# Performance work log

Hardware: AMD Instinct MI355X
Metric: run time of the kernel (lower is better)

## Reference

```python
import jax, jax.numpy as jnp
import numpy as np

E = 8          # num_global_experts (experts['count_per_node'])
D = 1024       # model_dim
H = 2048       # expert hidden_size
TOP_K = 2      # gate_type['k']


def setup_inputs() -> dict:
    key = jax.random.key(0)
    k_x, k_g, k_w1, k_w2 = jax.random.split(key, 4)
    B, S = 4, 2048
    inp = {
        "input": jax.random.normal(k_x, (B, S, D), dtype=jnp.float32),
        "Wg": jax.random.normal(k_g, (D, E), dtype=jnp.float32) * 0.02,
        "W1": jax.random.normal(k_w1, (E, D, H), dtype=jnp.float32) * 0.02,
        "b1": jnp.zeros((E, H), dtype=jnp.float32),
        "W2": jax.random.normal(k_w2, (E, H, D), dtype=jnp.float32) * 0.02,
        "b2": jnp.zeros((E, D), dtype=jnp.float32),
    }
    return inp


def reference(input, Wg, W1, b1, W2, b2):
    # ---- router: top-k softmax gating, gate weights normalized over top-k ----
    logits = jnp.einsum("bsd,de->bse", input, Wg)            # [B,S,E]
    probs = jax.nn.softmax(logits, axis=-1)                   # [B,S,E]
    top_vals, top_idx = jax.lax.top_k(probs, TOP_K)           # [B,S,K]
    top_vals = top_vals / jnp.sum(top_vals, axis=-1, keepdims=True)
    onehot = jax.nn.one_hot(top_idx, E, dtype=input.dtype)    # [B,S,K,E]
    mask = jnp.sum(onehot, axis=2)                            # [B,S,E] 0/1 dispatch mask (indices)
    scores = jnp.sum(onehot * top_vals[..., None], axis=2)    # [B,S,E] combine weights

    # ---- dense masked dispatch: repeat input per expert, mask non-routed tokens ----
    xm = input[None] * jnp.moveaxis(mask, -1, 0)[..., None]   # [E,B,S,D]

    # ---- per-expert 2-layer MLP (LinearExperts) ----
    h = jnp.einsum("ebsd,edh->ebsh", xm, W1) + b1[:, None, None, :]
    h = jax.nn.relu(h)                                        # [E,B,S,H]
    y = jnp.einsum("ebsh,ehd->ebsd", h, W2) + b2[:, None, None, :]

    # ---- weighted combine: sum_e expert_out * gate score ----
    out = jnp.sum(y * jnp.moveaxis(scores, -1, 0)[..., None], axis=0)  # [B,S,D]
    return out
```

## Files before the change

### kernel.cpp

```cpp
#include <hip/hip_runtime.h>
#include <hip/hip_bf16.h>

typedef __bf16 bf16x8 __attribute__((ext_vector_type(8)));
typedef __bf16 bf16x4 __attribute__((ext_vector_type(4)));
typedef float  f32x4  __attribute__((ext_vector_type(4)));

#define T_TOK    8192
#define D_DIM    1024
#define H_DIM    2048
#define E_NUM    8
#define MAX_MB   136
#define MAX_ROWS 17408

#define OFF_MBTOT   512
#define OFF_MB2E    1024
#define OFF_MBROW0  2048
#define OFF_TOPKE   4096
#define OFF_TOPKS   69632
#define OFF_TOK     135168
#define OFF_ROWIDX  204800
#define OFF_XB      (1u<<20)
#define OFF_W1T     (18u*1024*1024)
#define OFF_W2T     (50u*1024*1024)
#define OFF_HBUF    (82u*1024*1024)
#define OFF_YBUF    OFF_XB

__device__ __forceinline__ void gload_lds16(const void* g, void* l) {
    __builtin_amdgcn_global_load_lds(
        (const __attribute__((address_space(1))) void*)g,
        (__attribute__((address_space(3))) void*)l, 16, 0, 0);
}

__global__ __launch_bounds__(256) void k_router_cvt(
    const float* __restrict__ x, const float* __restrict__ Wg,
    __bf16* __restrict__ xb, int* __restrict__ topk_e, float* __restrict__ topk_s)
{
    __shared__ float wgT[E_NUM][1032];
    const int tid = threadIdx.x;
#pragma unroll
    for (int i = 0; i < 32; ++i) {
        int f = tid + i * 256;
        wgT[f & 7][f >> 3] = Wg[f];
    }
    __syncthreads();

    const int wave = tid >> 6, lane = tid & 63;
    const int t = blockIdx.x * 4 + wave;
    const float* xr = x + (size_t)t * D_DIM;
    __bf16* xbr = xb + (size_t)t * D_DIM;

    float acc[E_NUM];
#pragma unroll
    for (int e = 0; e < E_NUM; ++e) acc[e] = 0.f;

#pragma unroll
    for (int j = 0; j < 4; ++j) {
        const int d0 = lane * 4 + j * 256;
        float4 xv = *(const float4*)(xr + d0);
        bf16x4 o = { (__bf16)xv.x, (__bf16)xv.y, (__bf16)xv.z, (__bf16)xv.w };
        *(bf16x4*)(xbr + d0) = o;
#pragma unroll
        for (int e = 0; e < E_NUM; ++e) {
            float4 wv = *(const float4*)&wgT[e][d0];
            acc[e] += xv.x * wv.x + xv.y * wv.y + xv.z * wv.z + xv.w * wv.w;
        }
    }
#pragma unroll
    for (int off = 32; off >= 1; off >>= 1)
#pragma unroll
        for (int e = 0; e < E_NUM; ++e) acc[e] += __shfl_xor(acc[e], off, 64);

    if (lane == 0) {
        int e0 = 0; float v0 = acc[0];
#pragma unroll
        for (int e = 1; e < E_NUM; ++e) if (acc[e] > v0) { v0 = acc[e]; e0 = e; }
        int e1 = -1; float v1 = -1e30f;
#pragma unroll
        for (int e = 0; e < E_NUM; ++e) if (e != e0 && acc[e] > v1) { v1 = acc[e]; e1 = e; }
        float s0 = 1.f / (1.f + __expf(v1 - v0));
        float s1 = 1.f - s0;
        topk_e[t*2+0] = e0; topk_e[t*2+1] = e1;
        topk_s[t*2+0] = s0; topk_s[t*2+1] = s1;
    }
}

#define SORT_T 256
__global__ __launch_bounds__(512) void k_sort(
    const int* __restrict__ topk_e,
    int* __restrict__ mbTot, int* __restrict__ mb2e, int* __restrict__ mbrow0,
    int* __restrict__ tok, int* __restrict__ rowidx)
{
    __shared__ int lcnt[E_NUM][SORT_T];
    __shared__ int base[E_NUM];
    __shared__ int etot[E_NUM];
    const int tid = threadIdx.x;

    if (tid < SORT_T) {
#pragma unroll
        for (int e = 0; e < E_NUM; ++e) lcnt[e][tid] = 0;
    }
    __syncthreads();

    if (tid < SORT_T) {
        const int4* p = (const int4*)(topk_e + tid * 64);
#pragma unroll
        for (int i = 0; i < 16; ++i) {
            int4 v = p[i];
            lcnt[v.x][tid]++; lcnt[v.y][tid]++; lcnt[v.z][tid]++; lcnt[v.w][tid]++;
        }
    }
    __syncthreads();

    {
        const int w = tid >> 6, l = tid & 63;
        int v0 = lcnt[w][l*4+0], v1 = lcnt[w][l*4+1], v2 = lcnt[w][l*4+2], v3 = lcnt[w][l*4+3];
        int s = v0 + v1 + v2 + v3;
        int inc = s;
#pragma unroll
        for (int off = 1; off < 64; off <<= 1) {
            int o = __shfl_up(inc, off, 64);
            if (l >= off) inc += o;
        }
        int exc = inc - s;
        lcnt[w][l*4+0] = exc;
        lcnt[w][l*4+1] = exc + v0;
        lcnt[w][l*4+2] = exc + v0 + v1;
        lcnt[w][l*4+3] = exc + v0 + v1 + v2;
        if (l == 63) etot[w] = inc;
    }
    __syncthreads();

    if (tid == 0) {
        int row = 0, mb = 0;
        for (int e = 0; e < E_NUM; ++e) {
            base[e] = row;
            int nb = (etot[e] + 127) >> 7;
            for (int b = 0; b < nb; ++b) { mb2e[mb] = e; mbrow0[mb] = row + b*128; ++mb; }
            row += nb * 128;
        }
        mbTot[0] = mb;
    }
    __syncthreads();

    if (tid < SORT_T) {
#pragma unroll
        for (int e = 0; e < E_NUM; ++e) lcnt[e][tid] += base[e];
        const int4* p = (const int4*)(topk_e + tid * 64);
#pragma unroll
        for (int i = 0; i < 16; ++i) {
            int4 v = p[i];
            int j0 = tid * 64 + i * 4;
            int r;
            r = lcnt[v.x][tid]++; tok[r] = (j0+0) >> 1; rowidx[j0+0] = r;
            r = lcnt[v.y][tid]++; tok[r] = (j0+1) >> 1; rowidx[j0+1] = r;
            r = lcnt[v.z][tid]++; tok[r] = (j0+2) >> 1; rowidx[j0+2] = r;
            r = lcnt[v.w][tid]++; tok[r] = (j0+3) >> 1; rowidx[j0+3] = r;
        }
    }
}

__global__ __launch_bounds__(256) void k_transpose(
    const float* __restrict__ in, __bf16* __restrict__ out, int R, int C)
{
    __shared__ float tile[64][65];
    const int e = blockIdx.z;
    const float* inp = in + (size_t)e * R * C;
    __bf16* outp = out + (size_t)e * R * C;
    const int r0 = blockIdx.x * 64, c0 = blockIdx.y * 64;
    const int c = threadIdx.x & 63, rr = threadIdx.x >> 6;
#pragma unroll
    for (int i = 0; i < 16; ++i) {
        int r = rr + i * 4;
        tile[r][c] = inp[(size_t)(r0 + r) * C + c0 + c];
    }
    __syncthreads();
#pragma unroll
    for (int i = 0; i < 16; ++i) {
        int cc = rr + i * 4;
        outp[(size_t)(c0 + cc) * R + r0 + c] = (__bf16)tile[c][cc];
    }
}

__global__ __launch_bounds__(256) void k_gemm1(
    const __bf16* __restrict__ xb, const __bf16* __restrict__ W1T,
    const float* __restrict__ b1, const int* __restrict__ tok,
    const int* __restrict__ mb2e, const int* __restrict__ mbrow0,
    const int* __restrict__ mbTot, __bf16* __restrict__ hbuf)
{
    const int id   = blockIdx.x;
    const int xcd  = id & 7;
    const int j    = id >> 3;
    const int nblk = j & 15;
    const int mb   = (j >> 4) * 8 + xcd;
    if (mb >= *mbTot) return;
    const int e    = mb2e[mb];
    const int row0 = mbrow0[mb];
    const int n0   = nblk * 128;

    __shared__ __align__(16) char smem[16384];

    const int tid = threadIdx.x;
    const int w = tid >> 6, l = tid & 63;
    const int part = (l & 3) ^ ((l >> 3) & 3);

    const __bf16* Wb = W1T + (size_t)e * (size_t)(H_DIM * D_DIM);
    const __bf16* gA[2]; const __bf16* gB[2];
#pragma unroll
    for (int jj = 0; jj < 2; ++jj) {
        int rr = (w*2 + jj) * 16 + (l >> 2);
        int t  = tok[row0 + rr];
        gA[jj] = xb + (size_t)t * D_DIM + part * 8;
        gB[jj] = Wb + (size_t)(n0 + rr) * D_DIM + part * 8;
    }
    char* ldsA0 = smem + (w*2 + 0) * 1024;
    char* ldsA1 = smem + (w*2 + 1) * 1024;
    char* ldsB0 = smem + 8192 + (w*2 + 0) * 1024;
    char* ldsB1 = smem + 8192 + (w*2 + 1) * 1024;

    const int r = l & 15, q = l >> 4;
    const int wm = w & 1, wn = w >> 1;
    const int qx = (q ^ ((r >> 1) & 3)) * 16;

    f32x4 acc[4][4];
#pragma unroll
    for (int mi = 0; mi < 4; ++mi)
#pragma unroll
        for (int ni = 0; ni < 4; ++ni) acc[mi][ni] = (f32x4){0.f, 0.f, 0.f, 0.f};

    for (int k0 = 0; k0 < D_DIM; k0 += 32) {
        gload_lds16(gA[0] + k0, ldsA0);
        gload_lds16(gA[1] + k0, ldsA1);
        gload_lds16(gB[0] + k0, ldsB0);
        gload_lds16(gB[1] + k0, ldsB1);
        __syncthreads();

        bf16x8 av[4], bv[4];
#pragma unroll
        for (int mi = 0; mi < 4; ++mi)
            av[mi] = *(const bf16x8*)(smem + ((wm*64 + mi*16 + r) * 64 + qx));
#pragma unroll
        for (int ni = 0; ni < 4; ++ni)
            bv[ni] = *(const bf16x8*)(smem + 8192 + ((wn*64 + ni*16 + r) * 64 + qx));
#pragma unroll
        for (int mi = 0; mi < 4; ++mi)
#pragma unroll
            for (int ni = 0; ni < 4; ++ni)
                acc[mi][ni] = __builtin_amdgcn_mfma_f32_16x16x32_bf16(av[mi], bv[ni], acc[mi][ni], 0, 0, 0);
        __syncthreads();
    }

    const float* b1e = b1 + (size_t)e * H_DIM;
    float bb[4];
#pragma unroll
    for (int ni = 0; ni < 4; ++ni) bb[ni] = b1e[n0 + wn*64 + ni*16 + r];
#pragma unroll
    for (int mi = 0; mi < 4; ++mi)
#pragma unroll
        for (int reg = 0; reg < 4; ++reg) {
            int m = wm*64 + mi*16 + q*4 + reg;
            __bf16* hrow = hbuf + (size_t)(row0 + m) * H_DIM + n0 + wn*64;
#pragma unroll
            for (int ni = 0; ni < 4; ++ni) {
                float v = acc[mi][ni][reg] + bb[ni];
                hrow[ni*16 + r] = (__bf16)fmaxf(v, 0.f);
            }
        }
}

__global__ __launch_bounds__(256) void k_gemm2(
    const __bf16* __restrict__ hbuf, const __bf16* __restrict__ W2T,
    const float* __restrict__ b2, const int* __restrict__ mb2e,
    const int* __restrict__ mbrow0, const int* __restrict__ mbTot,
    __bf16* __restrict__ ybuf)
{
    const int id   = blockIdx.x;
    const int xcd  = id & 7;
    const int j    = id >> 3;
    const int nblk = j & 7;
    const int mb   = (j >> 3) * 8 + xcd;
    if (mb >= *mbTot) return;
    const int e    = mb2e[mb];
    const int row0 = mbrow0[mb];
    const int n0   = nblk * 128;

    __shared__ __align__(16) char smem[16384];

    const int tid = threadIdx.x;
    const int w = tid >> 6, l = tid & 63;
    const int part = (l & 3) ^ ((l >> 3) & 3);

    const __bf16* Wb = W2T + (size_t)e * (size_t)(D_DIM * H_DIM);
    const __bf16* gA[2]; const __bf16* gB[2];
#pragma unroll
    for (int jj = 0; jj < 2; ++jj) {
        int rr = (w*2 + jj) * 16 + (l >> 2);
        gA[jj] = hbuf + (size_t)(row0 + rr) * H_DIM + part * 8;
        gB[jj] = Wb + (size_t)(n0 + rr) * H_DIM + part * 8;
    }
    char* ldsA0 = smem + (w*2 + 0) * 1024;
    char* ldsA1 = smem + (w*2 + 1) * 1024;
    char* ldsB0 = smem + 8192 + (w*2 + 0) * 1024;
    char* ldsB1 = smem + 8192 + (w*2 + 1) * 1024;

    const int r = l & 15, q = l >> 4;
    const int wm = w & 1, wn = w >> 1;
    const int qx = (q ^ ((r >> 1) & 3)) * 16;

    f32x4 acc[4][4];
#pragma unroll
    for (int mi = 0; mi < 4; ++mi)
#pragma unroll
        for (int ni = 0; ni < 4; ++ni) acc[mi][ni] = (f32x4){0.f, 0.f, 0.f, 0.f};

    for (int k0 = 0; k0 < H_DIM; k0 += 32) {
        gload_lds16(gA[0] + k0, ldsA0);
        gload_lds16(gA[1] + k0, ldsA1);
        gload_lds16(gB[0] + k0, ldsB0);
        gload_lds16(gB[1] + k0, ldsB1);
        __syncthreads();

        bf16x8 av[4], bv[4];
#pragma unroll
        for (int mi = 0; mi < 4; ++mi)
            av[mi] = *(const bf16x8*)(smem + ((wm*64 + mi*16 + r) * 64 + qx));
#pragma unroll
        for (int ni = 0; ni < 4; ++ni)
            bv[ni] = *(const bf16x8*)(smem + 8192 + ((wn*64 + ni*16 + r) * 64 + qx));
#pragma unroll
        for (int mi = 0; mi < 4; ++mi)
#pragma unroll
            for (int ni = 0; ni < 4; ++ni)
                acc[mi][ni] = __builtin_amdgcn_mfma_f32_16x16x32_bf16(av[mi], bv[ni], acc[mi][ni], 0, 0, 0);
        __syncthreads();
    }

    const float* b2e = b2 + (size_t)e * D_DIM;
    float bb[4];
#pragma unroll
    for (int ni = 0; ni < 4; ++ni) bb[ni] = b2e[n0 + wn*64 + ni*16 + r];
#pragma unroll
    for (int mi = 0; mi < 4; ++mi)
#pragma unroll
        for (int reg = 0; reg < 4; ++reg) {
            int row = row0 + wm*64 + mi*16 + q*4 + reg;
            __bf16* yrow = ybuf + (size_t)row * D_DIM + n0 + wn*64;
#pragma unroll
            for (int ni = 0; ni < 4; ++ni)
                yrow[ni*16 + r] = (__bf16)(acc[mi][ni][reg] + bb[ni]);
        }
}

__global__ __launch_bounds__(256) void k_combine(
    const __bf16* __restrict__ ybuf, const int* __restrict__ rowidx,
    const float* __restrict__ topk_s, float* __restrict__ out)
{
    const int t = blockIdx.x;
    const int d0 = threadIdx.x * 4;
    const int r0 = rowidx[t*2+0], r1 = rowidx[t*2+1];
    const float s0 = topk_s[t*2+0], s1 = topk_s[t*2+1];
    bf16x4 y0 = *(const bf16x4*)(ybuf + (size_t)r0 * D_DIM + d0);
    bf16x4 y1 = *(const bf16x4*)(ybuf + (size_t)r1 * D_DIM + d0);
    float4 o;
    o.x = s0 * (float)y0[0] + s1 * (float)y1[0];
    o.y = s0 * (float)y0[1] + s1 * (float)y1[1];
    o.z = s0 * (float)y0[2] + s1 * (float)y1[2];
    o.w = s0 * (float)y0[3] + s1 * (float)y1[3];
    *(float4*)(out + (size_t)t * D_DIM + d0) = o;
}

extern "C" void kernel_launch(void* const* d_in, const int* in_sizes, int n_in,
                              void* d_out, int out_size, void* d_ws, size_t ws_size,
                              hipStream_t stream) {
    const float* x  = (const float*)d_in[0];
    const float* Wg = (const float*)d_in[1];
    const float* W1 = (const float*)d_in[2];
    const float* b1 = (const float*)d_in[3];
    const float* W2 = (const float*)d_in[4];
    const float* b2 = (const float*)d_in[5];
    float* out = (float*)d_out;
    char* ws = (char*)d_ws;

    int*   mbTot  = (int*)  (ws + OFF_MBTOT);
    int*   mb2e   = (int*)  (ws + OFF_MB2E);
    int*   mbrow0 = (int*)  (ws + OFF_MBROW0);
    int*   topk_e = (int*)  (ws + OFF_TOPKE);
    float* topk_s = (float*)(ws + OFF_TOPKS);
    int*   tok    = (int*)  (ws + OFF_TOK);
    int*   rowidx = (int*)  (ws + OFF_ROWIDX);
    __bf16* xb   = (__bf16*)(ws + OFF_XB);
    __bf16* W1T  = (__bf16*)(ws + OFF_W1T);
    __bf16* W2T  = (__bf16*)(ws + OFF_W2T);
    __bf16* hbuf = (__bf16*)(ws + OFF_HBUF);
    __bf16* ybuf = (__bf16*)(ws + OFF_YBUF);

    hipMemsetAsync(ws + OFF_TOK, 0, MAX_ROWS * sizeof(int), stream);

    k_router_cvt<<<T_TOK/4, 256, 0, stream>>>(x, Wg, xb, topk_e, topk_s);
    k_sort      <<<1, 512, 0, stream>>>(topk_e, mbTot, mb2e, mbrow0, tok, rowidx);
    k_transpose <<<dim3(D_DIM/64, H_DIM/64, E_NUM), 256, 0, stream>>>(W1, W1T, D_DIM, H_DIM);
    k_transpose <<<dim3(H_DIM/64, D_DIM/64, E_NUM), 256, 0, stream>>>(W2, W2T, H_DIM, D_DIM);

    k_gemm1<<<MAX_MB * (H_DIM/128), 256, 0, stream>>>(xb, W1T, b1, tok, mb2e, mbrow0, mbTot, hbuf);
    k_gemm2<<<MAX_MB * (D_DIM/128), 256, 0, stream>>>(hbuf, W2T, b2, mb2e, mbrow0, mbTot, ybuf);
    k_combine<<<T_TOK, 256, 0, stream>>>(ybuf, rowidx, topk_s, out);
}
```

Baseline: 424.3 us.

## Replace grouped GEMMs with 256x256-tile 8-wave pipelined double-buffered kernel

Replaces the two 128x128 single-buffered expert GEMM kernels with a templated 512-thread kernel using 256x256 output tiles, 128KB LDS double buffering, XOR-swizzled layout, and interleaved async global-to-LDS loads with MFMA phases under explicit waitcnt/barriers and priority hints. The sort kernel now emits 256-row macroblocks with per-block row ends, and epilogue stores are masked to valid rows. This aims to raise MFMA utilization and data reuse while hiding load latency. The risks are padding waste in partially filled 256-row blocks, fewer blocks in flight, and scheduling fragility.

```diff
diff --git a/kernel.cpp b/kernel.cpp
--- a/kernel.cpp
+++ b/kernel.cpp
@@ -9,12 +9,13 @@
 #define D_DIM    1024
 #define H_DIM    2048
 #define E_NUM    8
-#define MAX_MB   136
 #define MAX_ROWS 17408
+#define MAX_MB256 72
 
 #define OFF_MBTOT   512
 #define OFF_MB2E    1024
 #define OFF_MBROW0  2048
+#define OFF_MBEND   3072
 #define OFF_TOPKE   4096
 #define OFF_TOPKS   69632
 #define OFF_TOK     135168
@@ -88,7 +89,7 @@
 __global__ __launch_bounds__(512) void k_sort(
     const int* __restrict__ topk_e,
     int* __restrict__ mbTot, int* __restrict__ mb2e, int* __restrict__ mbrow0,
-    int* __restrict__ tok, int* __restrict__ rowidx)
+    int* __restrict__ mbrowEnd, int* __restrict__ tok, int* __restrict__ rowidx)
 {
     __shared__ int lcnt[E_NUM][SORT_T];
     __shared__ int base[E_NUM];
@@ -134,11 +135,20 @@
         int row = 0, mb = 0;
         for (int e = 0; e < E_NUM; ++e) {
             base[e] = row;
-            int nb = (etot[e] + 127) >> 7;
-            for (int b = 0; b < nb; ++b) { mb2e[mb] = e; mbrow0[mb] = row + b*128; ++mb; }
-            row += nb * 128;
+            int nb128 = (etot[e] + 127) >> 7;
+            int len   = nb128 << 7;
+            int nb    = (nb128 + 1) >> 1;
+            for (int b = 0; b < nb; ++b) {
+                mb2e[mb]   = e;
+                mbrow0[mb] = row + b * 256;
+                int re = row + len, be = row + b * 256 + 256;
+                mbrowEnd[mb] = re < be ? re : be;
+                ++mb;
+            }
+            row += len;
         }
         mbTot[0] = mb;
+        mbTot[1] = row;
     }
     __syncthreads();
 
@@ -181,172 +191,178 @@
     }
 }
 
-__global__ __launch_bounds__(256) void k_gemm1(
-    const __bf16* __restrict__ xb, const __bf16* __restrict__ W1T,
-    const float* __restrict__ b1, const int* __restrict__ tok,
+
+template<int BUF, int MIB>
+__device__ __forceinline__ void rd_av(const char* sm, int wm, int r, int q, bf16x8 (&av)[4][2]) {
+    const int rx = r & 7;
+    const char* ab = sm + BUF*32768 + wm*16384 + r*128;
+#pragma unroll
+    for (int m2 = 0; m2 < 4; ++m2) {
+        const char* rp = ab + (MIB*64 + m2*16)*128;
+        av[m2][0] = *(const bf16x8*)(rp + (((0|q) ^ rx) << 4));
+        av[m2][1] = *(const bf16x8*)(rp + (((4|q) ^ rx) << 4));
+    }
+}
+template<int BUF, int NIB>
+__device__ __forceinline__ void rd_bv(const char* sm, int wn, int r, int q, bf16x8 (&bv)[2][2][2]) {
+    const int rx = r & 7;
+    const char* bb = sm + 65536 + BUF*32768 + (wn>>1)*16384 + ((wn&1)*64 + NIB*32 + r)*128;
+#pragma unroll
+    for (int n2 = 0; n2 < 2; ++n2) {
+        const char* rp = bb + n2*16*128;
+        bv[NIB][n2][0] = *(const bf16x8*)(rp + (((0|q) ^ rx) << 4));
+        bv[NIB][n2][1] = *(const bf16x8*)(rp + (((4|q) ^ rx) << 4));
+    }
+}
+template<int MIB, int NIB>
+__device__ __forceinline__ void mfma16(const bf16x8 (&av)[4][2], const bf16x8 (&bv)[2][2][2],
+                                       f32x4 (&acc)[8][4]) {
+#pragma unroll
+    for (int m2 = 0; m2 < 4; ++m2)
+#pragma unroll
+        for (int n2 = 0; n2 < 2; ++n2) {
+            f32x4 c = acc[MIB*4+m2][NIB*2+n2];
+            c = __builtin_amdgcn_mfma_f32_16x16x32_bf16(av[m2][0], bv[NIB][n2][0], c, 0, 0, 0);
+            c = __builtin_amdgcn_mfma_f32_16x16x32_bf16(av[m2][1], bv[NIB][n2][1], c, 0, 0, 0);
+            acc[MIB*4+m2][NIB*2+n2] = c;
+        }
+}
+
+#define SBAR __builtin_amdgcn_sched_barrier(0)
+#define BARR __builtin_amdgcn_s_barrier()
+#define WLG  { asm volatile("s_waitcnt lgkmcnt(0)" ::: "memory"); SBAR; }
+#define WVM4 { asm volatile("s_waitcnt vmcnt(4)" ::: "memory"); SBAR; }
+#define WVM0 { asm volatile("s_waitcnt vmcnt(0)" ::: "memory"); SBAR; }
+#define P1 __builtin_amdgcn_s_setprio(1)
+#define P0 __builtin_amdgcn_s_setprio(0)
+#define STAGE_A(B_, H_, T_) { \
+    gload_lds16(pA[H_][0] + (T_)*64, smem + (B_)*32768 + (H_)*16384 + wq); \
+    gload_lds16(pA[H_][1] + (T_)*64, smem + (B_)*32768 + (H_)*16384 + 8192 + wq); }
+#define STAGE_B(B_, H_, T_) { \
+    gload_lds16(pB[H_][0] + (T_)*64, smem + 65536 + (B_)*32768 + (H_)*16384 + wq); \
+    gload_lds16(pB[H_][1] + (T_)*64, smem + 65536 + (B_)*32768 + (H_)*16384 + 8192 + wq); }
+
+template<int KD, int NBLK, bool GATHER, bool RELU>
+__global__ __launch_bounds__(512, 2) void k_gemm8(
+    const __bf16* __restrict__ Asrc, const __bf16* __restrict__ WT,
+    const float* __restrict__ bias, const int* __restrict__ tok,
     const int* __restrict__ mb2e, const int* __restrict__ mbrow0,
-    const int* __restrict__ mbTot, __bf16* __restrict__ hbuf)
+    const int* __restrict__ mbrowEnd, const int* __restrict__ mbTot,
+    __bf16* __restrict__ outp)
 {
+    constexpr int NT = KD / 64;
+    constexpr int NOUT = NBLK * 256;
+    __shared__ __align__(16) char smem[131072];
+
     const int id   = blockIdx.x;
     const int xcd  = id & 7;
     const int j    = id >> 3;
-    const int nblk = j & 15;
-    const int mb   = (j >> 4) * 8 + xcd;
-    if (mb >= *mbTot) return;
-    const int e    = mb2e[mb];
-    const int row0 = mbrow0[mb];
-    const int n0   = nblk * 128;
-
-    __shared__ __align__(16) char smem[16384];
+    const int nblk = j % NBLK;
+    const int mbi  = (j / NBLK) * 8 + xcd;
+    if (mbi >= mbTot[0]) return;
+    const int rowTot = mbTot[1];
+    const int e    = mb2e[mbi];
+    const int row0 = mbrow0[mbi];
+    const int rEnd = mbrowEnd[mbi];
+    const int n0   = nblk * 256;
 
     const int tid = threadIdx.x;
     const int w = tid >> 6, l = tid & 63;
-    const int part = (l & 3) ^ ((l >> 3) & 3);
-
-    const __bf16* Wb = W1T + (size_t)e * (size_t)(H_DIM * D_DIM);
-    const __bf16* gA[2]; const __bf16* gB[2];
-#pragma unroll
-    for (int jj = 0; jj < 2; ++jj) {
-        int rr = (w*2 + jj) * 16 + (l >> 2);
-        int t  = tok[row0 + rr];
-        gA[jj] = xb + (size_t)t * D_DIM + part * 8;
-        gB[jj] = Wb + (size_t)(n0 + rr) * D_DIM + part * 8;
-    }
-    char* ldsA0 = smem + (w*2 + 0) * 1024;
-    char* ldsA1 = smem + (w*2 + 1) * 1024;
-    char* ldsB0 = smem + 8192 + (w*2 + 0) * 1024;
-    char* ldsB1 = smem + 8192 + (w*2 + 1) * 1024;
-
     const int r = l & 15, q = l >> 4;
-    const int wm = w & 1, wn = w >> 1;
-    const int qx = (q ^ ((r >> 1) & 3)) * 16;
-
-    f32x4 acc[4][4];
-#pragma unroll
-    for (int mi = 0; mi < 4; ++mi)
+    const int wm = w >> 2, wn = w & 3;
+    const int wq = w * 1024;
+
+    const int Rrow = l >> 3;
+    const int cg   = (l & 7) ^ Rrow;
+    const __bf16* Wb = WT + (size_t)e * ((size_t)NOUT * KD);
+    const __bf16* pA[2][2]; const __bf16* pB[2][2];
+#pragma unroll
+    for (int h = 0; h < 2; ++h)
+#pragma unroll
+        for (int s = 0; s < 2; ++s) {
+            int R  = s*64 + w*8 + Rrow;
+            int ra = row0 + h*128 + R;
+            ra = ra < rowTot ? ra : (rowTot - 1);
+            if (GATHER) pA[h][s] = Asrc + (size_t)tok[ra] * KD + cg*8;
+            else        pA[h][s] = Asrc + (size_t)ra * KD + cg*8;
+            pB[h][s] = Wb + (size_t)(n0 + h*128 + R) * KD + cg*8;
+        }
+
+    f32x4 acc[8][4];
+#pragma unroll
+    for (int mi = 0; mi < 8; ++mi)
 #pragma unroll
         for (int ni = 0; ni < 4; ++ni) acc[mi][ni] = (f32x4){0.f, 0.f, 0.f, 0.f};
 
-    for (int k0 = 0; k0 < D_DIM; k0 += 32) {
-        gload_lds16(gA[0] + k0, ldsA0);
-        gload_lds16(gA[1] + k0, ldsA1);
-        gload_lds16(gB[0] + k0, ldsB0);
-        gload_lds16(gB[1] + k0, ldsB1);
-        __syncthreads();
-
-        bf16x8 av[4], bv[4];
-#pragma unroll
-        for (int mi = 0; mi < 4; ++mi)
-            av[mi] = *(const bf16x8*)(smem + ((wm*64 + mi*16 + r) * 64 + qx));
-#pragma unroll
-        for (int ni = 0; ni < 4; ++ni)
-            bv[ni] = *(const bf16x8*)(smem + 8192 + ((wn*64 + ni*16 + r) * 64 + qx));
-#pragma unroll
-        for (int mi = 0; mi < 4; ++mi)
-#pragma unroll
-            for (int ni = 0; ni < 4; ++ni)
-                acc[mi][ni] = __builtin_amdgcn_mfma_f32_16x16x32_bf16(av[mi], bv[ni], acc[mi][ni], 0, 0, 0);
-        __syncthreads();
-    }
-
-    const float* b1e = b1 + (size_t)e * H_DIM;
-    float bb[4];
-#pragma unroll
-    for (int ni = 0; ni < 4; ++ni) bb[ni] = b1e[n0 + wn*64 + ni*16 + r];
-#pragma unroll
-    for (int mi = 0; mi < 4; ++mi)
+    bf16x8 av[4][2];
+    bf16x8 bv[2][2][2];
+
+    STAGE_B(0,0,0); STAGE_B(0,1,0); STAGE_A(0,0,0); STAGE_A(0,1,0);
+    STAGE_B(1,0,1); STAGE_B(1,1,1);
+    WVM4; BARR; SBAR;
+
+    for (int t0 = 0; t0 < NT - 2; t0 += 2) {
+        rd_av<0,0>(smem, wm, r, q, av); rd_bv<0,0>(smem, wn, r, q, bv);
+        STAGE_A(1,0,t0+1);
+        SBAR; BARR; WLG; P1; mfma16<0,0>(av, bv, acc); P0; BARR; SBAR;
+        rd_bv<0,1>(smem, wn, r, q, bv);
+        STAGE_A(1,1,t0+1);
+        SBAR; BARR; WLG; P1; mfma16<0,1>(av, bv, acc); P0; BARR; SBAR;
+        rd_av<0,1>(smem, wm, r, q, av);
+        STAGE_B(0,0,t0+2);
+        SBAR; BARR; WLG; P1; mfma16<1,0>(av, bv, acc); P0; BARR; SBAR;
+        STAGE_B(0,1,t0+2);
+        SBAR; BARR; WLG; P1; mfma16<1,1>(av, bv, acc); P0; WVM4; BARR; SBAR;
+        rd_av<1,0>(smem, wm, r, q, av); rd_bv<1,0>(smem, wn, r, q, bv);
+        STAGE_A(0,0,t0+2);
+        SBAR; BARR; WLG; P1; mfma16<0,0>(av, bv, acc); P0; BARR; SBAR;
+        rd_bv<1,1>(smem, wn, r, q, bv);
+        STAGE_A(0,1,t0+2);
+        SBAR; BARR; WLG; P1; mfma16<0,1>(av, bv, acc); P0; BARR; SBAR;
+        rd_av<1,1>(smem, wm, r, q, av);
+        STAGE_B(1,0,t0+3);
+        SBAR; BARR; WLG; P1; mfma16<1,0>(av, bv, acc); P0; BARR; SBAR;
+        STAGE_B(1,1,t0+3);
+        SBAR; BARR; WLG; P1; mfma16<1,1>(av, bv, acc); P0; WVM4; BARR; SBAR;
+    }
+    {
+        const int t0 = NT - 2;
+        rd_av<0,0>(smem, wm, r, q, av); rd_bv<0,0>(smem, wn, r, q, bv);
+        STAGE_A(1,0,t0+1);
+        SBAR; BARR; WLG; P1; mfma16<0,0>(av, bv, acc); P0; BARR; SBAR;
+        rd_bv<0,1>(smem, wn, r, q, bv);
+        STAGE_A(1,1,t0+1);
+        SBAR; BARR; WLG; P1; mfma16<0,1>(av, bv, acc); P0; BARR; SBAR;
+        rd_av<0,1>(smem, wm, r, q, av);
+        SBAR; BARR; WLG; P1; mfma16<1,0>(av, bv, acc); P0; BARR; SBAR;
+        SBAR; BARR; WLG; P1; mfma16<1,1>(av, bv, acc); P0; WVM0; BARR; SBAR;
+        rd_av<1,0>(smem, wm, r, q, av); rd_bv<1,0>(smem, wn, r, q, bv);
+        SBAR; BARR; WLG; P1; mfma16<0,0>(av, bv, acc); P0; BARR; SBAR;
+        rd_bv<1,1>(smem, wn, r, q, bv);
+        SBAR; BARR; WLG; P1; mfma16<0,1>(av, bv, acc); P0; BARR; SBAR;
+        rd_av<1,1>(smem, wm, r, q, av);
+        SBAR; BARR; WLG; P1; mfma16<1,0>(av, bv, acc); P0; BARR; SBAR;
+        SBAR; BARR; WLG; P1; mfma16<1,1>(av, bv, acc); P0; BARR; SBAR;
+    }
+
+    const float* be = bias + (size_t)e * NOUT;
+    float bb4[4];
+#pragma unroll
+    for (int n2 = 0; n2 < 4; ++n2) bb4[n2] = be[n0 + wn*64 + n2*16 + r];
+#pragma unroll
+    for (int mi = 0; mi < 8; ++mi)
 #pragma unroll
         for (int reg = 0; reg < 4; ++reg) {
-            int m = wm*64 + mi*16 + q*4 + reg;
-            __bf16* hrow = hbuf + (size_t)(row0 + m) * H_DIM + n0 + wn*64;
-#pragma unroll
-            for (int ni = 0; ni < 4; ++ni) {
-                float v = acc[mi][ni][reg] + bb[ni];
-                hrow[ni*16 + r] = (__bf16)fmaxf(v, 0.f);
+            int row = row0 + wm*128 + mi*16 + q*4 + reg;
+            if (row < rEnd) {
+                __bf16* orow = outp + (size_t)row * NOUT + n0 + wn*64;
+#pragma unroll
+                for (int n2 = 0; n2 < 4; ++n2) {
+                    float v = acc[mi][n2][reg] + bb4[n2];
+                    if (RELU) v = fmaxf(v, 0.f);
+                    orow[n2*16 + r] = (__bf16)v;
+                }
             }
-        }
-}
-
-__global__ __launch_bounds__(256) void k_gemm2(
-    const __bf16* __restrict__ hbuf, const __bf16* __restrict__ W2T,
-    const float* __restrict__ b2, const int* __restrict__ mb2e,
-    const int* __restrict__ mbrow0, const int* __restrict__ mbTot,
-    __bf16* __restrict__ ybuf)
-{
-    const int id   = blockIdx.x;
-    const int xcd  = id & 7;
-    const int j    = id >> 3;
-    const int nblk = j & 7;
-    const int mb   = (j >> 3) * 8 + xcd;
-    if (mb >= *mbTot) return;
-    const int e    = mb2e[mb];
-    const int row0 = mbrow0[mb];
-    const int n0   = nblk * 128;
-
-    __shared__ __align__(16) char smem[16384];
-
-    const int tid = threadIdx.x;
-    const int w = tid >> 6, l = tid & 63;
-    const int part = (l & 3) ^ ((l >> 3) & 3);
-
-    const __bf16* Wb = W2T + (size_t)e * (size_t)(D_DIM * H_DIM);
-    const __bf16* gA[2]; const __bf16* gB[2];
-#pragma unroll
-    for (int jj = 0; jj < 2; ++jj) {
-        int rr = (w*2 + jj) * 16 + (l >> 2);
-        gA[jj] = hbuf + (size_t)(row0 + rr) * H_DIM + part * 8;
-        gB[jj] = Wb + (size_t)(n0 + rr) * H_DIM + part * 8;
-    }
-    char* ldsA0 = smem + (w*2 + 0) * 1024;
-    char* ldsA1 = smem + (w*2 + 1) * 1024;
-    char* ldsB0 = smem + 8192 + (w*2 + 0) * 1024;
-    char* ldsB1 = smem + 8192 + (w*2 + 1) * 1024;
-
-    const int r = l & 15, q = l >> 4;
-    const int wm = w & 1, wn = w >> 1;
-    const int qx = (q ^ ((r >> 1) & 3)) * 16;
-
-    f32x4 acc[4][4];
-#pragma unroll
-    for (int mi = 0; mi < 4; ++mi)
-#pragma unroll
-        for (int ni = 0; ni < 4; ++ni) acc[mi][ni] = (f32x4){0.f, 0.f, 0.f, 0.f};
-
-    for (int k0 = 0; k0 < H_DIM; k0 += 32) {
-        gload_lds16(gA[0] + k0, ldsA0);
-        gload_lds16(gA[1] + k0, ldsA1);
-        gload_lds16(gB[0] + k0, ldsB0);
-        gload_lds16(gB[1] + k0, ldsB1);
-        __syncthreads();
-
-        bf16x8 av[4], bv[4];
-#pragma unroll
-        for (int mi = 0; mi < 4; ++mi)
-            av[mi] = *(const bf16x8*)(smem + ((wm*64 + mi*16 + r) * 64 + qx));
-#pragma unroll
-        for (int ni = 0; ni < 4; ++ni)
-            bv[ni] = *(const bf16x8*)(smem + 8192 + ((wn*64 + ni*16 + r) * 64 + qx));
-#pragma unroll
-        for (int mi = 0; mi < 4; ++mi)
-#pragma unroll
-            for (int ni = 0; ni < 4; ++ni)
-                acc[mi][ni] = __builtin_amdgcn_mfma_f32_16x16x32_bf16(av[mi], bv[ni], acc[mi][ni], 0, 0, 0);
-        __syncthreads();
-    }
-
-    const float* b2e = b2 + (size_t)e * D_DIM;
-    float bb[4];
-#pragma unroll
-    for (int ni = 0; ni < 4; ++ni) bb[ni] = b2e[n0 + wn*64 + ni*16 + r];
-#pragma unroll
-    for (int mi = 0; mi < 4; ++mi)
-#pragma unroll
-        for (int reg = 0; reg < 4; ++reg) {
-            int row = row0 + wm*64 + mi*16 + q*4 + reg;
-            __bf16* yrow = ybuf + (size_t)row * D_DIM + n0 + wn*64;
-#pragma unroll
-            for (int ni = 0; ni < 4; ++ni)
-                yrow[ni*16 + r] = (__bf16)(acc[mi][ni][reg] + bb[ni]);
         }
 }
 
@@ -383,6 +399,7 @@
     int*   mbTot  = (int*)  (ws + OFF_MBTOT);
     int*   mb2e   = (int*)  (ws + OFF_MB2E);
     int*   mbrow0 = (int*)  (ws + OFF_MBROW0);
+    int*   mbrowEnd = (int*)(ws + OFF_MBEND);
     int*   topk_e = (int*)  (ws + OFF_TOPKE);
     float* topk_s = (float*)(ws + OFF_TOPKS);
     int*   tok    = (int*)  (ws + OFF_TOK);
@@ -396,11 +413,14 @@
     hipMemsetAsync(ws + OFF_TOK, 0, MAX_ROWS * sizeof(int), stream);
 
     k_router_cvt<<<T_TOK/4, 256, 0, stream>>>(x, Wg, xb, topk_e, topk_s);
-    k_sort      <<<1, 512, 0, stream>>>(topk_e, mbTot, mb2e, mbrow0, tok, rowidx);
+    k_sort      <<<1, 512, 0, stream>>>(topk_e, mbTot, mb2e, mbrow0, mbrowEnd, tok, rowidx);
     k_transpose <<<dim3(D_DIM/64, H_DIM/64, E_NUM), 256, 0, stream>>>(W1, W1T, D_DIM, H_DIM);
     k_transpose <<<dim3(H_DIM/64, D_DIM/64, E_NUM), 256, 0, stream>>>(W2, W2T, H_DIM, D_DIM);
 
-    k_gemm1<<<MAX_MB * (H_DIM/128), 256, 0, stream>>>(xb, W1T, b1, tok, mb2e, mbrow0, mbTot, hbuf);
-    k_gemm2<<<MAX_MB * (D_DIM/128), 256, 0, stream>>>(hbuf, W2T, b2, mb2e, mbrow0, mbTot, ybuf);
+    k_gemm8<D_DIM, H_DIM/256, true,  true ><<<MAX_MB256 * (H_DIM/256), 512, 0, stream>>>(
+        xb, W1T, b1, tok, mb2e, mbrow0, mbrowEnd, mbTot, hbuf);
+    k_gemm8<H_DIM, D_DIM/256, false, false><<<MAX_MB256 * (D_DIM/256), 512, 0, stream>>>(
+        hbuf, W2T, b2, tok, mb2e, mbrow0, mbrowEnd, mbTot, ybuf);
+
     k_combine<<<T_TOK, 256, 0, stream>>>(ybuf, rowidx, topk_s, out);
 }
```

Result: slower. 447.7 us (+5.5%).
